# Optimization experiments

Hardware: AMD Instinct MI355X
Metric: run time of the kernel (lower is better)

Reference implementation:

```python
import jax, jax.numpy as jnp
import numpy as np

B, S, D, Fd, M, H, L = 4, 1024, 1024, 4096, 512, 16, 2
HD = D // H
EPS = 1e-5


def _ln(x, s, b):
    m = jnp.mean(x, axis=-1, keepdims=True)
    v = jnp.mean((x - m) ** 2, axis=-1, keepdims=True)
    return (x - m) * jax.lax.rsqrt(v + EPS) * s + b


def _mha(x, Wq, bq, Wk, bk, Wv, bv, Wo, bo):
    b_, s_, _ = x.shape
    Q = (x @ Wq + bq).reshape(b_, s_, H, HD)
    K = (x @ Wk + bk).reshape(b_, s_, H, HD)
    V = (x @ Wv + bv).reshape(b_, s_, H, HD)
    scores = jnp.einsum('bihd,bjhd->bhij', Q, K) / np.sqrt(HD).astype(np.float32)
    w = jax.nn.softmax(scores, axis=-1)
    out = jnp.einsum('bhij,bjhd->bihd', w, V).reshape(b_, s_, D)
    return out @ Wo + bo


def setup_inputs() -> dict:
    key = jax.random.key(0)
    ks = iter(jax.random.split(key, 40))
    w = lambda shape: jax.random.normal(next(ks), shape, jnp.float32) * 0.02
    inp = {
        'x': jax.random.normal(next(ks), (B, S, D), jnp.float32),
        # stacked per-global-layer params [L, ...]
        'Wq': w((L, D, D)), 'bq': jnp.zeros((L, D)),
        'Wk': w((L, D, D)), 'bk': jnp.zeros((L, D)),
        'Wv': w((L, D, D)), 'bv': jnp.zeros((L, D)),
        'Wo': w((L, D, D)), 'bo': jnp.zeros((L, D)),
        'W1': w((L, D, Fd)), 'b1': jnp.zeros((L, Fd)),
        'W2': w((L, Fd, D)), 'b2': jnp.zeros((L, D)),
        'n1s': jnp.ones((L, D)), 'n1b': jnp.zeros((L, D)),
        'n2s': jnp.ones((L, D)), 'n2b': jnp.zeros((L, D)),
        # top-level params
        'ln1s': jnp.ones((D,)), 'ln1b': jnp.zeros((D,)),
        'ln2s': jnp.ones((D,)), 'ln2b': jnp.zeros((D,)),
        'ln3s': jnp.ones((D,)), 'ln3b': jnp.zeros((D,)),
        'Wb': w((D, M)), 'bb': jnp.zeros((M,)),      # backbone stand-in
        'Wm': w((M, D)), 'bm': jnp.zeros((D,)),      # self.linear
        'Wf1': w((D, Fd)), 'bf1': jnp.zeros((Fd,)),  # top feed_forward
        'Wf2': w((Fd, D)), 'bf2': jnp.zeros((D,)),
    }
    return inp


def reference(x, Wq, bq, Wk, bk, Wv, bv, Wo, bo, W1, b1, W2, b2,
              n1s, n1b, n2s, n2b, ln1s, ln1b, ln2s, ln2b, ln3s, ln3b,
              Wb, bb, Wm, bm, Wf1, bf1, Wf2, bf2):
    # dropout is identity (eval mode)
    # global branch: stacked EncoderLayers
    g = x
    for i in range(L):
        a = _mha(g, Wq[i], bq[i], Wk[i], bk[i], Wv[i], bv[i], Wo[i], bo[i])
        g = _ln(g + a, n1s[i], n1b[i])
        ff = jax.nn.relu(g @ W1[i] + b1[i]) @ W2[i] + b2[i]
        g = _ln(g + ff, n2s[i], n2b[i])

    def local(frac):
        st = S // frac
        xs = x[:, -st:, :]
        mo = (xs @ Wb + bb) @ Wm + bm
        y = _ln(xs + mo, ln1s, ln1b)
        return jnp.pad(y, ((0, 0), (S - st, 0), (0, 0)))

    output = g + local(2) + local(4)  # S >= 4 branch
    h = _ln(output + x, ln2s, ln2b)
    ff = jax.nn.relu(output @ Wf1 + bf1) @ Wf2 + bf2
    return _ln(h + ff, ln3s, ln3b)
```

## Files before the change

### kernel.cpp

```cpp
#include <hip/hip_runtime.h>
#include <stdint.h>


typedef short   s16x8 __attribute__((ext_vector_type(8)));
typedef float   f32x4 __attribute__((ext_vector_type(4)));
typedef uint16_t u16x8 __attribute__((ext_vector_type(8)));
typedef uint16_t u16x4 __attribute__((ext_vector_type(4)));

__device__ __forceinline__ float bf2f(uint16_t h) {
    union { uint32_t u; float f; } c; c.u = ((uint32_t)h) << 16; return c.f;
}
__device__ __forceinline__ uint16_t f2bf(float f) {
    union { float f; uint32_t u; } c; c.f = f;
    uint32_t u = c.u;
    u += 0x7fffu + ((u >> 16) & 1u);
    return (uint16_t)(u >> 16);
}

__device__ __forceinline__ void g2l16(const uint16_t* g, uint16_t* l) {
    __builtin_amdgcn_global_load_lds(
        (const __attribute__((address_space(1))) void*)g,
        (__attribute__((address_space(3))) void*)l, 16, 0, 0);
}

template<int MODE>
__global__ __launch_bounds__(256, 2) void gemm128n(
    const uint16_t* __restrict__ A, const uint16_t* __restrict__ Bt,
    const float* __restrict__ bias0, const float* __restrict__ bias1,
    const float* __restrict__ bias2,
    uint16_t* __restrict__ C0, uint16_t* __restrict__ C1,
    uint16_t* __restrict__ C2,
    int N)
{
    __shared__ __align__(16) uint16_t smem[36864];
    uint16_t* sA = smem;
    uint16_t* sB = smem + 12288;

    const int t    = threadIdx.x;
    const int w    = t >> 6;
    const int lane = t & 63;
    const int qd   = lane >> 4;
    const int cc   = lane & 15;
    const int wn   = w * 64;

    const int id  = blockIdx.x;
    const int loc = id >> 3;
    const int bm  = (id & 7) * 4 + (loc & 3);
    const int bn  = loc >> 2;
    const int m0  = bm * 128;
    const int n0  = bn * 256;

    const float* bp = bias0;
    int n0c = n0;
    if (MODE == 3) {
        int seg = n0 >> 10;
        n0c = n0 & 1023;
        bp = (seg == 0) ? bias0 : (seg == 1) ? bias1 : bias2;
    }
    float bb[4];
#pragma unroll
    for (int j = 0; j < 4; ++j) bb[j] = bp[n0c + wn + j * 16 + cc];

    int offA[8], offB[4];
#pragma unroll
    for (int i = 0; i < 8; ++i) {
        int ml = i * 16 + cc;
        offA[i] = ml * 32 + ((qd ^ ((ml >> 1) & 3)) * 8);
    }
#pragma unroll
    for (int j = 0; j < 4; ++j) {
        int nl = wn + j * 16 + cc;
        offB[j] = nl * 32 + ((qd ^ ((nl >> 1) & 3)) * 8);
    }

    const uint16_t* pA[2]; int ldA[2];
#pragma unroll
    for (int is = 0; is < 2; ++is) {
        int gc = is * 256 + t;
        int row = gc >> 2, ph = gc & 3;
        pA[is]  = A + (size_t)(m0 + row) * 1024 + (ph ^ ((row >> 1) & 3)) * 8;
        ldA[is] = (is * 256 + w * 64) * 8;
    }
    const uint16_t* pB[4]; int ldB[4];
#pragma unroll
    for (int is = 0; is < 4; ++is) {
        int gc = is * 256 + t;
        int row = gc >> 2, ph = gc & 3;
        pB[is]  = Bt + (size_t)(n0 + row) * 1024 + (ph ^ ((row >> 1) & 3)) * 8;
        ldB[is] = (is * 256 + w * 64) * 8;
    }
    auto stage = [&](int tt, int slot) {
        int kt = tt * 32;
        uint16_t* dA = sA + slot * 4096;
        uint16_t* dB = sB + slot * 8192;
#pragma unroll
        for (int is = 0; is < 2; ++is) g2l16(pA[is] + kt, dA + ldA[is]);
#pragma unroll
        for (int is = 0; is < 4; ++is) g2l16(pB[is] + kt, dB + ldB[is]);
    };

    f32x4 acc[8][4];
#pragma unroll
    for (int i = 0; i < 8; ++i)
#pragma unroll
        for (int j = 0; j < 4; ++j) acc[i][j] = (f32x4)0.0f;

    stage(0, 0); stage(1, 1);
    asm volatile("s_waitcnt vmcnt(6)" ::: "memory");
    __builtin_amdgcn_s_barrier();

    int cur = 0, pf = 2;
#pragma unroll 1
    for (int kt = 0; kt < 32; ++kt) {
        const uint16_t* sa = sA + cur * 4096;
        const uint16_t* sb = sB + cur * 8192;
        s16x8 av[8], bv[4];
#pragma unroll
        for (int j = 0; j < 4; ++j) bv[j] = *(const s16x8*)(sb + offB[j]);
#pragma unroll
        for (int i = 0; i < 8; ++i) av[i] = *(const s16x8*)(sa + offA[i]);
        if (kt < 30) stage(kt + 2, pf);
        asm volatile("s_waitcnt lgkmcnt(0)" ::: "memory");
        __builtin_amdgcn_sched_barrier(0);
        __builtin_amdgcn_s_setprio(1);
#pragma unroll
        for (int i = 0; i < 8; ++i)
#pragma unroll
            for (int j = 0; j < 4; ++j)
                acc[i][j] = __builtin_amdgcn_mfma_f32_16x16x32_bf16(
                    av[i], bv[j], acc[i][j], 0, 0, 0);
        __builtin_amdgcn_s_setprio(0);
        if (kt < 30)       { asm volatile("s_waitcnt vmcnt(6)" ::: "memory"); }
        else if (kt == 30) { asm volatile("s_waitcnt vmcnt(0)" ::: "memory"); }
        __builtin_amdgcn_s_barrier();
        pf = cur;
        cur = (cur == 2) ? 0 : cur + 1;
    }

    if (MODE == 3 && (n0 >> 10) == 2) {
#pragma unroll
        for (int j = 0; j < 4; ++j) {
            int c = n0c + wn + j * 16 + cc;
            int hh = c >> 6, d = c & 63;
#pragma unroll
            for (int i = 0; i < 8; ++i) {
                int rb = m0 + i * 16 + qd * 4;
                int b = rb >> 10, s = rb & 1023;
                u16x4 o;
#pragma unroll
                for (int r = 0; r < 4; ++r) o[r] = f2bf(acc[i][j][r] + bb[j]);
                *(u16x4*)(C2 + ((size_t)((b * 16 + hh) * 64 + d)) * 1024 + s) = o;
            }
        }
        return;
    }
    {
        uint16_t* C = C0;
        int Nc = N;
        if (MODE == 3) {
            int seg = n0 >> 10;
            C = (seg == 0) ? C0 : C1;
            Nc = 1024;
        }
        constexpr int ST = 264;
#pragma unroll
        for (int i = 0; i < 8; ++i)
#pragma unroll
            for (int j = 0; j < 4; ++j) {
                f32x4 v = acc[i][j];
#pragma unroll
                for (int r = 0; r < 4; ++r) {
                    float val = v[r] + bb[j];
                    if (MODE == 1) val = fmaxf(val, 0.0f);
                    smem[(i * 16 + qd * 4 + r) * ST + wn + j * 16 + cc] = f2bf(val);
                }
            }
        __syncthreads();
#pragma unroll
        for (int p = 0; p < 16; ++p) {
            int row  = p * 8 + (t >> 5);
            int colc = (t & 31) * 8;
            u16x8 v = *(const u16x8*)(smem + row * ST + colc);
            *(u16x8*)(C + (size_t)(m0 + row) * Nc + n0c + colc) = v;
        }
    }
}

template<int MODE, int BN, int BK, int DB>
__global__ __launch_bounds__(256) void gemm_bt(
    const uint16_t* __restrict__ A, const uint16_t* __restrict__ Bt,
    const float* __restrict__ bias0, const float* __restrict__ bias1,
    const float* __restrict__ bias2,
    uint16_t* __restrict__ C0, uint16_t* __restrict__ C1,
    uint16_t* __restrict__ C2,
    int M, int N, int K)
{
    constexpr int JN   = BN / 32;
    constexpr int KS   = BK / 32;
    constexpr int CPR  = BK / 8;
    constexpr int LG   = (BK == 32) ? 2 : 3;
    constexpr int RA   = (128 * BK / 8) / 256;
    constexpr int RB   = (BN  * BK / 8) / 256;
    constexpr int NBUF = DB ? 2 : 1;
    constexpr int STG  = NBUF * (128 + BN) * BK;
    constexpr int EPI  = (MODE == 3) ? 0 : 128 * (BN + 8);
    constexpr int SMEM = (STG > EPI) ? STG : EPI;
    __shared__ __align__(16) uint16_t smem[SMEM];
    uint16_t* sAp = smem;
    uint16_t* sBp = smem + NBUF * 128 * BK;

    const int t    = threadIdx.x;
    const int w    = t >> 6;
    const int lane = t & 63;
    const int qd   = lane >> 4;
    const int cc   = lane & 15;

    int bm, bn;
    {
        int gx = gridDim.x, gy = gridDim.y;
        if ((gy & 7) == 0) {
            int id   = blockIdx.y * gx + blockIdx.x;
            int gpg  = gy >> 3;
            int rest = id >> 3;
            bm = (id & 7) * gpg + rest % gpg;
            bn = rest / gpg;
        } else { bm = blockIdx.y; bn = blockIdx.x; }
    }
    const int m0 = bm * 128;
    const int n0 = bn * BN;
    const int wm = (w >> 1) * 64;
    const int wn = (w & 1) * (BN / 2);

    auto key = [](int row) -> int {
        return (BK == 32) ? ((row >> 1) & 3) : (row & 7);
    };

    f32x4 acc[4][JN];
#pragma unroll
    for (int i = 0; i < 4; ++i)
#pragma unroll
        for (int j = 0; j < JN; ++j) acc[i][j] = (f32x4)0.0f;

    int rA[RA], kA[RA];
#pragma unroll
    for (int is = 0; is < RA; ++is) {
        int gc = is * 256 + t;
        int row = gc >> LG, ph = gc & (CPR - 1);
        rA[is] = row;
        kA[is] = (ph ^ key(row)) * 8;
    }
    int rB[RB], kB[RB];
#pragma unroll
    for (int is = 0; is < RB; ++is) {
        int gc = is * 256 + t;
        int row = gc >> LG, ph = gc & (CPR - 1);
        rB[is] = row;
        kB[is] = (ph ^ key(row)) * 8;
    }
    int offA[4][KS], offB[JN][KS];
#pragma unroll
    for (int i = 0; i < 4; ++i) {
        int ml = wm + i * 16 + cc;
#pragma unroll
        for (int ks = 0; ks < KS; ++ks)
            offA[i][ks] = ml * BK + ((ks * 4 + qd) ^ key(ml)) * 8;
    }
#pragma unroll
    for (int j = 0; j < JN; ++j) {
        int nl = wn + j * 16 + cc;
#pragma unroll
        for (int ks = 0; ks < KS; ++ks)
            offB[j][ks] = nl * BK + ((ks * 4 + qd) ^ key(nl)) * 8;
    }

    auto stage = [&](int kt, int buf) {
#pragma unroll
        for (int is = 0; is < RA; ++is)
            g2l16(A + (size_t)(m0 + rA[is]) * K + kt + kA[is],
                  sAp + (size_t)buf * 128 * BK + (size_t)(is * 256 + w * 64) * 8);
#pragma unroll
        for (int is = 0; is < RB; ++is)
            g2l16(Bt + (size_t)(n0 + rB[is]) * K + kt + kB[is],
                  sBp + (size_t)buf * BN * BK + (size_t)(is * 256 + w * 64) * 8);
    };
    auto compute = [&](int buf) {
        const uint16_t* sa = sAp + (size_t)buf * 128 * BK;
        const uint16_t* sb = sBp + (size_t)buf * BN * BK;
#pragma unroll
        for (int ks = 0; ks < KS; ++ks) {
            s16x8 af[4], bv[JN];
#pragma unroll
            for (int i = 0; i < 4; ++i) af[i] = *(const s16x8*)(sa + offA[i][ks]);
#pragma unroll
            for (int j = 0; j < JN; ++j) bv[j] = *(const s16x8*)(sb + offB[j][ks]);
#pragma unroll
            for (int i = 0; i < 4; ++i)
#pragma unroll
                for (int j = 0; j < JN; ++j)
                    acc[i][j] = __builtin_amdgcn_mfma_f32_16x16x32_bf16(
                        af[i], bv[j], acc[i][j], 0, 0, 0);
        }
    };

    if (DB) {
        stage(0, 0);
        __syncthreads();
        int cur = 0;
        for (int kt = 0; kt < K; kt += BK) {
            if (kt + BK < K) stage(kt + BK, cur ^ 1);
            compute(cur);
            __syncthreads();
            cur ^= 1;
        }
    } else {
        for (int kt = 0; kt < K; kt += BK) {
            stage(kt, 0);
            __syncthreads();
            compute(0);
            __syncthreads();
        }
    }

    if (MODE == 3) {
#pragma unroll
        for (int j = 0; j < JN; ++j) {
            int col = n0 + wn + j * 16 + cc;
            int seg = col >> 10;
            const float* bp = (seg == 0) ? bias0 : (seg == 1) ? bias1 : bias2;
            float bb = bp[col & 1023];
#pragma unroll
            for (int i = 0; i < 4; ++i) {
                f32x4 v = acc[i][j];
#pragma unroll
                for (int r = 0; r < 4; ++r) {
                    float val = v[r] + bb;
                    int row = m0 + wm + i * 16 + qd * 4 + r;
                    if (col < 1024) {
                        C0[(size_t)row * 1024 + col] = f2bf(val);
                    } else if (col < 2048) {
                        C1[(size_t)row * 1024 + (col - 1024)] = f2bf(val);
                    } else {
                        int c = col - 2048;
                        int b = row >> 10, s = row & 1023;
                        int hh = c >> 6, d = c & 63;
                        C2[((size_t)(b * 16 + hh) * 64 + d) * 1024 + s] = f2bf(val);
                    }
                }
            }
        }
    } else {
        constexpr int ST = BN + 8;
#pragma unroll
        for (int j = 0; j < JN; ++j) {
            int col = wn + j * 16 + cc;
            float bb = bias0[n0 + col];
#pragma unroll
            for (int i = 0; i < 4; ++i) {
                f32x4 v = acc[i][j];
#pragma unroll
                for (int r = 0; r < 4; ++r) {
                    float val = v[r] + bb;
                    if (MODE == 1) val = fmaxf(val, 0.0f);
                    smem[(wm + i * 16 + qd * 4 + r) * ST + col] = f2bf(val);
                }
            }
        }
        __syncthreads();
        constexpr int NP  = 128 * BN / 2048;
        constexpr int TPR = BN / 8;
#pragma unroll
        for (int p = 0; p < NP; ++p) {
            int row  = p * (256 / TPR) + t / TPR;
            int colc = (t % TPR) * 8;
            u16x8 v = *(const u16x8*)(smem + row * ST + colc);
            *(u16x8*)(C0 + (size_t)(m0 + row) * N + n0 + colc) = v;
        }
    }
}

#define FA_P 76
__global__ __launch_bounds__(256) void flash_attn(
    const uint16_t* __restrict__ Q, const uint16_t* __restrict__ K,
    const uint16_t* __restrict__ Vt, uint16_t* __restrict__ O)
{
    __shared__ __align__(16) uint16_t Qs[64 * FA_P];
    __shared__ __align__(16) uint16_t Ks[64 * FA_P];
    __shared__ __align__(16) uint16_t Vs[64 * FA_P];
    __shared__ __align__(16) uint16_t Ps[64 * FA_P];

    const int t    = threadIdx.x;
    const int w    = t >> 6;
    const int lane = t & 63;
    const int qd   = lane >> 4;
    const int cc   = lane & 15;
    const int id   = blockIdx.x;
    const int xg   = id & 7;
    const int loc  = id >> 3;
    const int bh   = xg * 8 + (loc >> 4);
    const int qblk = loc & 15;
    const int b    = bh >> 4, hh = bh & 15;
    const size_t rowbase = (size_t)b * 1024;

#pragma unroll
    for (int is = 0; is < 2; ++is) {
        int c = is * 256 + t, r = c >> 3, ch = c & 7;
        *(u16x8*)(Qs + r * FA_P + ch * 8) =
            *(const u16x8*)(Q + (rowbase + qblk * 64 + r) * 1024 + hh * 64 + ch * 8);
    }

    f32x4 o[4];
    float lrow[4] = {0.0f, 0.0f, 0.0f, 0.0f};
#pragma unroll
    for (int j = 0; j < 4; ++j) o[j] = (f32x4)0.0f;

    for (int kb = 0; kb < 1024; kb += 64) {
        __syncthreads();
#pragma unroll
        for (int is = 0; is < 2; ++is) {
            int c = is * 256 + t, r = c >> 3, ch = c & 7;
            *(u16x8*)(Ks + r * FA_P + ch * 8) =
                *(const u16x8*)(K + (rowbase + kb + r) * 1024 + hh * 64 + ch * 8);
            *(u16x8*)(Vs + r * FA_P + ch * 8) =
                *(const u16x8*)(Vt + ((size_t)(bh * 64 + r)) * 1024 + kb + ch * 8);
        }
        __syncthreads();

        f32x4 sc[4];
        s16x8 aq0 = *(const s16x8*)(Qs + (w * 16 + cc) * FA_P + qd * 8);
        s16x8 aq1 = *(const s16x8*)(Qs + (w * 16 + cc) * FA_P + 32 + qd * 8);
#pragma unroll
        for (int j = 0; j < 4; ++j) {
            s16x8 b0 = *(const s16x8*)(Ks + (j * 16 + cc) * FA_P + qd * 8);
            s16x8 b1 = *(const s16x8*)(Ks + (j * 16 + cc) * FA_P + 32 + qd * 8);
            sc[j] = __builtin_amdgcn_mfma_f32_16x16x32_bf16(aq0, b0, (f32x4)0.0f, 0, 0, 0);
            sc[j] = __builtin_amdgcn_mfma_f32_16x16x32_bf16(aq1, b1, sc[j], 0, 0, 0);
        }

#pragma unroll
        for (int r = 0; r < 4; ++r) {
            float p0 = __expf(sc[0][r] * 0.125f);
            float p1 = __expf(sc[1][r] * 0.125f);
            float p2 = __expf(sc[2][r] * 0.125f);
            float p3 = __expf(sc[3][r] * 0.125f);
            lrow[r] += (p0 + p1) + (p2 + p3);
            int prow = (w * 16 + qd * 4 + r) * FA_P + cc;
            Ps[prow]      = f2bf(p0);
            Ps[prow + 16] = f2bf(p1);
            Ps[prow + 32] = f2bf(p2);
            Ps[prow + 48] = f2bf(p3);
        }

#pragma unroll
        for (int ks = 0; ks < 2; ++ks) {
            s16x8 ap = *(const s16x8*)(Ps + (w * 16 + cc) * FA_P + ks * 32 + qd * 8);
#pragma unroll
            for (int j = 0; j < 4; ++j) {
                s16x8 bb = *(const s16x8*)(Vs + (j * 16 + cc) * FA_P + ks * 32 + qd * 8);
                o[j] = __builtin_amdgcn_mfma_f32_16x16x32_bf16(ap, bb, o[j], 0, 0, 0);
            }
        }
    }

#pragma unroll
    for (int r = 0; r < 4; ++r) {
        float rs = lrow[r];
        rs += __shfl_xor(rs, 1);
        rs += __shfl_xor(rs, 2);
        rs += __shfl_xor(rs, 4);
        rs += __shfl_xor(rs, 8);
        float inv = 1.0f / rs;
        size_t grow = rowbase + qblk * 64 + w * 16 + qd * 4 + r;
#pragma unroll
        for (int j = 0; j < 4; ++j)
            O[grow * 1024 + hh * 64 + j * 16 + cc] = f2bf(o[j][r] * inv);
    }
}

template<int BT, int F32OUT>
__global__ __launch_bounds__(256) void ln_res(
    const uint16_t* __restrict__ A, const void* __restrict__ Bp,
    const float* __restrict__ S, const float* __restrict__ Bi,
    void* __restrict__ outp)
{
    const int row = blockIdx.x, t = threadIdx.x;
    const int w = t >> 6, lane = t & 63;
    u16x4 a4 = *(const u16x4*)(A + (size_t)row * 1024 + t * 4);
    float bvals[4];
    if (BT == 0) {
        u16x4 b4 = *(const u16x4*)((const uint16_t*)Bp + (size_t)row * 1024 + t * 4);
#pragma unroll
        for (int e = 0; e < 4; ++e) bvals[e] = bf2f(b4[e]);
    } else {
        float4 b4 = *(const float4*)((const float*)Bp + (size_t)row * 1024 + t * 4);
        bvals[0] = b4.x; bvals[1] = b4.y; bvals[2] = b4.z; bvals[3] = b4.w;
    }
    float v[4], sum = 0.0f, sq = 0.0f;
#pragma unroll
    for (int e = 0; e < 4; ++e) {
        v[e] = bf2f(a4[e]) + bvals[e];
        sum += v[e];
        sq  += v[e] * v[e];
    }
#pragma unroll
    for (int d = 1; d < 64; d <<= 1) {
        sum += __shfl_xor(sum, d);
        sq  += __shfl_xor(sq, d);
    }
    __shared__ float rs[4], rq[4];
    if (lane == 0) { rs[w] = sum; rq[w] = sq; }
    __syncthreads();
    sum = rs[0] + rs[1] + rs[2] + rs[3];
    sq  = rq[0] + rq[1] + rq[2] + rq[3];
    float mean = sum * (1.0f / 1024.0f);
    float var  = sq * (1.0f / 1024.0f) - mean * mean;
    float rstd = rsqrtf(var + 1e-5f);
    float4 s4  = *(const float4*)(S + t * 4);
    float4 bi4 = *(const float4*)(Bi + t * 4);
    float r0 = (v[0] - mean) * rstd * s4.x + bi4.x;
    float r1 = (v[1] - mean) * rstd * s4.y + bi4.y;
    float r2 = (v[2] - mean) * rstd * s4.z + bi4.z;
    float r3 = (v[3] - mean) * rstd * s4.w + bi4.w;
    if (F32OUT) {
        *(float4*)((float*)outp + (size_t)row * 1024 + t * 4) =
            make_float4(r0, r1, r2, r3);
    } else {
        u16x4 o4;
        o4[0] = f2bf(r0); o4[1] = f2bf(r1); o4[2] = f2bf(r2); o4[3] = f2bf(r3);
        *(u16x4*)((uint16_t*)outp + (size_t)row * 1024 + t * 4) = o4;
    }
}

__global__ __launch_bounds__(256) void add3(
    const uint16_t* __restrict__ g, const uint16_t* __restrict__ y2,
    const uint16_t* __restrict__ y4, uint16_t* __restrict__ out)
{
    size_t e = ((size_t)blockIdx.x * 256 + threadIdx.x) * 4;
    int row = (int)(e >> 10), col = (int)(e & 1023);
    int b = row >> 10, s = row & 1023;
    u16x4 gv = *(const u16x4*)(g + e);
    float v[4];
#pragma unroll
    for (int k = 0; k < 4; ++k) v[k] = bf2f(gv[k]);
    if (s >= 512) {
        u16x4 a = *(const u16x4*)(y2 + ((size_t)(b * 512 + s - 512)) * 1024 + col);
#pragma unroll
        for (int k = 0; k < 4; ++k) v[k] += bf2f(a[k]);
    }
    if (s >= 768) {
        u16x4 a = *(const u16x4*)(y4 + ((size_t)(b * 256 + s - 768)) * 1024 + col);
#pragma unroll
        for (int k = 0; k < 4; ++k) v[k] += bf2f(a[k]);
    }
    u16x4 o4;
#pragma unroll
    for (int k = 0; k < 4; ++k) o4[k] = f2bf(v[k]);
    *(u16x4*)(out + e) = o4;
}

__global__ __launch_bounds__(256) void copy_rows_f32(
    const float* __restrict__ x, uint16_t* __restrict__ out, int lgst)
{
    size_t e = ((size_t)blockIdx.x * 256 + threadIdx.x) * 4;
    int row = (int)(e >> 10), col = (int)(e & 1023);
    int st = 1 << lgst;
    int b = row >> lgst, s = row & (st - 1);
    float4 a = *(const float4*)(x + ((size_t)(b * 1024 + (1024 - st) + s)) * 1024 + col);
    u16x4 o4;
    o4[0] = f2bf(a.x); o4[1] = f2bf(a.y); o4[2] = f2bf(a.z); o4[3] = f2bf(a.w);
    *(u16x4*)(out + e) = o4;
}

__global__ __launch_bounds__(256) void transpose_k(
    const float* __restrict__ W, uint16_t* __restrict__ Wt, int Kd, int Nd)
{
    __shared__ uint16_t tile[64][68];
    const int t  = threadIdx.x;
    const int n0 = blockIdx.x * 64, k0 = blockIdx.y * 64;
#pragma unroll
    for (int p = 0; p < 4; ++p) {
        int k  = p * 16 + (t >> 4);
        int nn = (t & 15) * 4;
        float4 a = *(const float4*)(W + (size_t)(k0 + k) * Nd + n0 + nn);
        tile[nn + 0][k] = f2bf(a.x);
        tile[nn + 1][k] = f2bf(a.y);
        tile[nn + 2][k] = f2bf(a.z);
        tile[nn + 3][k] = f2bf(a.w);
    }
    __syncthreads();
#pragma unroll
    for (int p = 0; p < 2; ++p) {
        int nn = p * 32 + (t >> 3);
        int kk = (t & 7) * 8;
        u16x8 o = *(const u16x8*)(&tile[nn][kk]);
        *(u16x8*)(Wt + (size_t)(n0 + nn) * Kd + k0 + kk) = o;
    }
}

__global__ __launch_bounds__(256) void cvt(
    const float* __restrict__ src, uint16_t* __restrict__ dst)
{
    size_t i = ((size_t)blockIdx.x * 256 + threadIdx.x) * 8;
    float4 a = *(const float4*)(src + i);
    float4 b = *(const float4*)(src + i + 4);
    u16x8 o;
    o[0] = f2bf(a.x); o[1] = f2bf(a.y); o[2] = f2bf(a.z); o[3] = f2bf(a.w);
    o[4] = f2bf(b.x); o[5] = f2bf(b.y); o[6] = f2bf(b.z); o[7] = f2bf(b.w);
    *(u16x8*)(dst + i) = o;
}

extern "C" void kernel_launch(void* const* d_in, const int* in_sizes, int n_in,
                              void* d_out, int out_size, void* d_ws, size_t ws_size,
                              hipStream_t stream)
{
    const float* x    = (const float*)d_in[0];
    const float* Wq   = (const float*)d_in[1];
    const float* bq   = (const float*)d_in[2];
    const float* Wk   = (const float*)d_in[3];
    const float* bk   = (const float*)d_in[4];
    const float* Wv   = (const float*)d_in[5];
    const float* bv   = (const float*)d_in[6];
    const float* Wo   = (const float*)d_in[7];
    const float* bo   = (const float*)d_in[8];
    const float* W1   = (const float*)d_in[9];
    const float* b1   = (const float*)d_in[10];
    const float* W2   = (const float*)d_in[11];
    const float* b2   = (const float*)d_in[12];
    const float* n1s  = (const float*)d_in[13];
    const float* n1b  = (const float*)d_in[14];
    const float* n2s  = (const float*)d_in[15];
    const float* n2b  = (const float*)d_in[16];
    const float* ln1s = (const float*)d_in[17];
    const float* ln1b = (const float*)d_in[18];
    const float* ln2s = (const float*)d_in[19];
    const float* ln2b = (const float*)d_in[20];
    const float* ln3s = (const float*)d_in[21];
    const float* ln3b = (const float*)d_in[22];
    const float* Wb   = (const float*)d_in[23];
    const float* bb   = (const float*)d_in[24];
    const float* Wm   = (const float*)d_in[25];
    const float* bm   = (const float*)d_in[26];
    const float* Wf1  = (const float*)d_in[27];
    const float* bf1  = (const float*)d_in[28];
    const float* Wf2  = (const float*)d_in[29];
    const float* bf2  = (const float*)d_in[30];

    char* ws = (char*)d_ws;
    const size_t MB = (size_t)1 << 20;
    uint16_t* g    = (uint16_t*)(ws);
    uint16_t* tb   = (uint16_t*)(ws + 8 * MB);
    char*     big  = ws + 16 * MB;
    uint16_t* qb   = (uint16_t*)(big);
    uint16_t* kbuf = (uint16_t*)(big + 8 * MB);
    uint16_t* vtb  = (uint16_t*)(big + 16 * MB);
    uint16_t* ob   = (uint16_t*)(big + 24 * MB);
    uint16_t* ffb  = (uint16_t*)(big);
    uint16_t* xbf  = (uint16_t*)(ws + 48 * MB);
    uint16_t* hb   = (uint16_t*)(ws + 48 * MB);
    uint16_t* wT   = (uint16_t*)(ws + 56 * MB);

    auto T = [&](const float* Wsrc, int Kd, int Nd, uint16_t* dst) {
        transpose_k<<<dim3(Nd / 64, Kd / 64), 256, 0, stream>>>(Wsrc, dst, Kd, Nd);
    };

    cvt<<<2048, 256, 0, stream>>>(x, xbf);

    const uint16_t* gin = xbf;
    for (int i = 0; i < 2; ++i) {
        const size_t wOff = (size_t)i * 1024 * 1024;
        const size_t fOff = (size_t)i * 1024 * 4096;
        T(Wq + wOff, 1024, 1024, wT);
        T(Wk + wOff, 1024, 1024, wT + (size_t)1024 * 1024);
        T(Wv + wOff, 1024, 1024, wT + (size_t)2048 * 1024);
        gemm128n<3><<<384, 256, 0, stream>>>(
            gin, wT, bq + i * 1024, bk + i * 1024, bv + i * 1024,
            qb, kbuf, vtb, 3072);
        flash_attn<<<1024, 256, 0, stream>>>(qb, kbuf, vtb, ob);
        T(Wo + wOff, 1024, 1024, wT);
        gemm_bt<0, 64, 64, 1><<<dim3(16, 32), 256, 0, stream>>>(
            ob, wT, bo + i * 1024, nullptr, nullptr, tb, nullptr, nullptr,
            4096, 1024, 1024);
        ln_res<0, 0><<<4096, 256, 0, stream>>>(gin, tb, n1s + i * 1024, n1b + i * 1024, g);
        T(W1 + fOff, 1024, 4096, wT);
        gemm128n<1><<<512, 256, 0, stream>>>(
            g, wT, b1 + i * 4096, nullptr, nullptr, ffb, nullptr, nullptr, 4096);
        T(W2 + fOff, 4096, 1024, wT);
        gemm_bt<0, 64, 64, 1><<<dim3(16, 32), 256, 0, stream>>>(
            ffb, wT, b2 + i * 1024, nullptr, nullptr, tb, nullptr, nullptr,
            4096, 1024, 4096);
        ln_res<0, 0><<<4096, 256, 0, stream>>>(g, tb, n2s + i * 1024, n2b + i * 1024, g);
        gin = g;
    }

    uint16_t* xsc = (uint16_t*)(big);
    uint16_t* lk  = (uint16_t*)(big + 8 * MB);
    uint16_t* mo  = (uint16_t*)(big + 16 * MB);
    uint16_t* yy  = (uint16_t*)(big + 24 * MB);
    copy_rows_f32<<<2048, 256, 0, stream>>>(x, xsc, 9);
    copy_rows_f32<<<1024, 256, 0, stream>>>(x, xsc + (size_t)2048 * 1024, 8);
    uint16_t* WbT = wT;
    uint16_t* WmT = wT + (size_t)512 * 1024;
    T(Wb, 1024, 512, WbT);
    T(Wm, 512, 1024, WmT);
    gemm_bt<0, 64, 64, 1><<<dim3(8, 24), 256, 0, stream>>>(
        xsc, WbT, bb, nullptr, nullptr, lk, nullptr, nullptr, 3072, 512, 1024);
    gemm_bt<0, 64, 64, 1><<<dim3(16, 24), 256, 0, stream>>>(
        lk, WmT, bm, nullptr, nullptr, mo, nullptr, nullptr, 3072, 1024, 512);
    ln_res<0, 0><<<3072, 256, 0, stream>>>(xsc, mo, ln1s, ln1b, yy);
    uint16_t* y2 = yy;
    uint16_t* y4 = yy + (size_t)2048 * 1024;

    add3<<<4096, 256, 0, stream>>>(g, y2, y4, g);
    ln_res<1, 0><<<4096, 256, 0, stream>>>(g, x, ln2s, ln2b, hb);
    T(Wf1, 1024, 4096, wT);
    gemm128n<1><<<512, 256, 0, stream>>>(
        g, wT, bf1, nullptr, nullptr, ffb, nullptr, nullptr, 4096);
    T(Wf2, 4096, 1024, wT);
    gemm_bt<0, 64, 64, 1><<<dim3(16, 32), 256, 0, stream>>>(
        ffb, wT, bf2, nullptr, nullptr, tb, nullptr, nullptr, 4096, 1024, 4096);
    ln_res<0, 1><<<4096, 256, 0, stream>>>(hb, tb, ln3s, ln3b, d_out);
}
```

Before: 762.6 us.

## Register-prefetch K/V tiles in flash attention and hoist Q fragments

The flash attention loop now loads the next K/V tile from global memory into registers while the current tile is being computed, then stores it to LDS at the top of the next iteration. Q fragments are read into registers once before the loop, and their LDS buffer is reused for P, which cuts shared memory use. P is converted to bf16 with the packed v_cvt_pk_bf16_f32 instruction instead of the manual rounding routine. The cost is extra registers for the prefetched tiles. Attention is only one part of the whole model's time.

```diff
diff --git a/kernel.cpp b/kernel.cpp
--- a/kernel.cpp
+++ b/kernel.cpp
@@ -15,6 +15,11 @@
     uint32_t u = c.u;
     u += 0x7fffu + ((u >> 16) & 1u);
     return (uint16_t)(u >> 16);
+}
+__device__ __forceinline__ uint32_t cvt_pk_bf16(float lo, float hi) {
+    uint32_t r;
+    asm("v_cvt_pk_bf16_f32 %0, %1, %2" : "=v"(r) : "v"(lo), "v"(hi));
+    return r;
 }
 
 __device__ __forceinline__ void g2l16(const uint16_t* g, uint16_t* l) {
@@ -383,10 +388,9 @@
     const uint16_t* __restrict__ Q, const uint16_t* __restrict__ K,
     const uint16_t* __restrict__ Vt, uint16_t* __restrict__ O)
 {
-    __shared__ __align__(16) uint16_t Qs[64 * FA_P];
+    __shared__ __align__(16) uint16_t QPs[64 * FA_P];
     __shared__ __align__(16) uint16_t Ks[64 * FA_P];
     __shared__ __align__(16) uint16_t Vs[64 * FA_P];
-    __shared__ __align__(16) uint16_t Ps[64 * FA_P];
 
     const int t    = threadIdx.x;
     const int w    = t >> 6;
@@ -401,33 +405,57 @@
     const int b    = bh >> 4, hh = bh & 15;
     const size_t rowbase = (size_t)b * 1024;
 
+    int rr[2], ch8[2], lws[2];
+    const uint16_t* Kp[2];
+    const uint16_t* Vp[2];
 #pragma unroll
     for (int is = 0; is < 2; ++is) {
-        int c = is * 256 + t, r = c >> 3, ch = c & 7;
-        *(u16x8*)(Qs + r * FA_P + ch * 8) =
-            *(const u16x8*)(Q + (rowbase + qblk * 64 + r) * 1024 + hh * 64 + ch * 8);
-    }
+        int c   = is * 256 + t;
+        rr[is]  = c >> 3;
+        ch8[is] = (c & 7) * 8;
+        lws[is] = rr[is] * FA_P + ch8[is];
+        Kp[is]  = K  + (rowbase + rr[is]) * 1024 + hh * 64 + ch8[is];
+        Vp[is]  = Vt + ((size_t)(bh * 64 + rr[is])) * 1024 + ch8[is];
+    }
+
+    u16x8 kr[2], vr[2];
+#pragma unroll
+    for (int is = 0; is < 2; ++is) {
+        kr[is] = *(const u16x8*)(Kp[is]);
+        vr[is] = *(const u16x8*)(Vp[is]);
+    }
+
+#pragma unroll
+    for (int is = 0; is < 2; ++is)
+        *(u16x8*)(QPs + lws[is]) =
+            *(const u16x8*)(Q + (rowbase + qblk * 64 + rr[is]) * 1024 + hh * 64 + ch8[is]);
+    __syncthreads();
+    s16x8 aq0 = *(const s16x8*)(QPs + (w * 16 + cc) * FA_P + qd * 8);
+    s16x8 aq1 = *(const s16x8*)(QPs + (w * 16 + cc) * FA_P + 32 + qd * 8);
+    __syncthreads();
 
     f32x4 o[4];
     float lrow[4] = {0.0f, 0.0f, 0.0f, 0.0f};
 #pragma unroll
     for (int j = 0; j < 4; ++j) o[j] = (f32x4)0.0f;
 
-    for (int kb = 0; kb < 1024; kb += 64) {
+#pragma unroll 1
+    for (int kb = 64; kb <= 1024; kb += 64) {
+#pragma unroll
+        for (int is = 0; is < 2; ++is) {
+            *(u16x8*)(Ks + lws[is]) = kr[is];
+            *(u16x8*)(Vs + lws[is]) = vr[is];
+        }
+        if (kb < 1024) {
+#pragma unroll
+            for (int is = 0; is < 2; ++is) {
+                kr[is] = *(const u16x8*)(Kp[is] + (size_t)kb * 1024);
+                vr[is] = *(const u16x8*)(Vp[is] + kb);
+            }
+        }
         __syncthreads();
-#pragma unroll
-        for (int is = 0; is < 2; ++is) {
-            int c = is * 256 + t, r = c >> 3, ch = c & 7;
-            *(u16x8*)(Ks + r * FA_P + ch * 8) =
-                *(const u16x8*)(K + (rowbase + kb + r) * 1024 + hh * 64 + ch * 8);
-            *(u16x8*)(Vs + r * FA_P + ch * 8) =
-                *(const u16x8*)(Vt + ((size_t)(bh * 64 + r)) * 1024 + kb + ch * 8);
-        }
-        __syncthreads();
 
         f32x4 sc[4];
-        s16x8 aq0 = *(const s16x8*)(Qs + (w * 16 + cc) * FA_P + qd * 8);
-        s16x8 aq1 = *(const s16x8*)(Qs + (w * 16 + cc) * FA_P + 32 + qd * 8);
 #pragma unroll
         for (int j = 0; j < 4; ++j) {
             s16x8 b0 = *(const s16x8*)(Ks + (j * 16 + cc) * FA_P + qd * 8);
@@ -444,21 +472,24 @@
             float p3 = __expf(sc[3][r] * 0.125f);
             lrow[r] += (p0 + p1) + (p2 + p3);
             int prow = (w * 16 + qd * 4 + r) * FA_P + cc;
-            Ps[prow]      = f2bf(p0);
-            Ps[prow + 16] = f2bf(p1);
-            Ps[prow + 32] = f2bf(p2);
-            Ps[prow + 48] = f2bf(p3);
+            uint32_t pk01 = cvt_pk_bf16(p0, p1);
+            uint32_t pk23 = cvt_pk_bf16(p2, p3);
+            QPs[prow]      = (uint16_t)pk01;
+            QPs[prow + 16] = (uint16_t)(pk01 >> 16);
+            QPs[prow + 32] = (uint16_t)pk23;
+            QPs[prow + 48] = (uint16_t)(pk23 >> 16);
         }
 
 #pragma unroll
         for (int ks = 0; ks < 2; ++ks) {
-            s16x8 ap = *(const s16x8*)(Ps + (w * 16 + cc) * FA_P + ks * 32 + qd * 8);
+            s16x8 ap = *(const s16x8*)(QPs + (w * 16 + cc) * FA_P + ks * 32 + qd * 8);
 #pragma unroll
             for (int j = 0; j < 4; ++j) {
-                s16x8 bb = *(const s16x8*)(Vs + (j * 16 + cc) * FA_P + ks * 32 + qd * 8);
-                o[j] = __builtin_amdgcn_mfma_f32_16x16x32_bf16(ap, bb, o[j], 0, 0, 0);
+                s16x8 bv = *(const s16x8*)(Vs + (j * 16 + cc) * FA_P + ks * 32 + qd * 8);
+                o[j] = __builtin_amdgcn_mfma_f32_16x16x32_bf16(ap, bv, o[j], 0, 0, 0);
             }
         }
+        __syncthreads();
     }
 
 #pragma unroll
```

Result: no change. 764.7 us (+0.3%).
